# Kernel optimization log

Measured on AMD Instinct MI355X. Metric: run time of the kernel, lower is better.

The kernel has to match this reference:

```python
import jax, jax.numpy as jnp
import numpy as np

B, M, D, E, T, K = 16384, 6, 128, 6, 60, 2

def _gelu(x):
    return jax.nn.gelu(x, approximate=False)  # torch default exact GELU

def setup_inputs() -> dict:
    key = jax.random.key(0)
    ks = jax.random.split(key, 20)
    def p(k, shape, fan_in):
        return (jax.random.normal(k, shape, jnp.float32) / np.sqrt(fan_in)).astype(jnp.float32)
    inp = {
        "mode_features": jax.random.normal(ks[0], (B, M, D), jnp.float32),
        # router MLP: D->256->128->E
        "rW1": p(ks[1], (D, 256), D),   "rb1": jnp.zeros((256,), jnp.float32),
        "rW2": p(ks[2], (256, 128), 256), "rb2": jnp.zeros((128,), jnp.float32),
        "rW3": p(ks[3], (128, E), 128), "rb3": jnp.zeros((E,), jnp.float32),
        # stacked expert trajectory heads: D->256->256->T*2
        "tW1": p(ks[4], (E, D, 256), D),   "tb1": jnp.zeros((E, 256), jnp.float32),
        "tW2": p(ks[5], (E, 256, 256), 256), "tb2": jnp.zeros((E, 256), jnp.float32),
        "tW3": p(ks[6], (E, 256, T * 2), 256), "tb3": jnp.zeros((E, T * 2), jnp.float32),
        # stacked expert score heads: D->128->64->1
        "sW1": p(ks[7], (E, D, 128), D),  "sb1": jnp.zeros((E, 128), jnp.float32),
        "sW2": p(ks[8], (E, 128, 64), 128), "sb2": jnp.zeros((E, 64), jnp.float32),
        "sW3": p(ks[9], (E, 64, 1), 64), "sb3": jnp.zeros((E, 1), jnp.float32),
    }
    return inp

def reference(mode_features, rW1, rb1, rW2, rb2, rW3, rb3,
              tW1, tb1, tW2, tb2, tW3, tb3,
              sW1, sb1, sW2, sb2, sW3, sb3):
    b, m, d = mode_features.shape
    x = mode_features.reshape(b * m, d)  # [N, D]

    # Router (dropout is inference no-op)
    h = _gelu(x @ rW1 + rb1)
    h = _gelu(h @ rW2 + rb2)
    logits = (h @ rW3 + rb3).reshape(b, m, E)
    probs = jax.nn.softmax(logits, axis=-1)  # [B, M, E]

    # Top-2 sparse gating
    top_v, top_i = jax.lax.top_k(logits, K)          # [B, M, K]
    top_w = jax.nn.softmax(top_v, axis=-1)           # renormalized over top-k
    sparse_w = jnp.sum(jax.nn.one_hot(top_i, E, dtype=top_w.dtype) * top_w[..., None], axis=2)  # [B, M, E]

    # All-expert trajectory heads (dense redundant compute, as in source)
    ht = _gelu(jnp.einsum('nd,edh->neh', x, tW1) + tb1)
    ht = _gelu(jnp.einsum('neh,ehk->nek', ht, tW2) + tb2)
    traj = (jnp.einsum('nek,eko->neo', ht, tW3) + tb3).reshape(b, m, E, T, 2)

    # All-expert score heads
    hs = _gelu(jnp.einsum('nd,edh->neh', x, sW1) + sb1)
    hs = _gelu(jnp.einsum('neh,ehk->nek', hs, sW2) + sb2)
    score = (jnp.einsum('nek,eko->neo', hs, sW3) + sb3)[..., 0].reshape(b, m, E)

    trajectories = jnp.einsum('bmeto,bme->bmto', traj, sparse_w)  # [B, M, T, 2]
    scores = jnp.einsum('bme,bme->bm', score, sparse_w)           # [B, M]

    avg = probs.reshape(b * m, E).mean(axis=0)
    aux_loss = E * jnp.sum(avg * avg)
    return trajectories, scores, aux_loss, probs
```

## Files before the change

### kernel.cpp

```cpp
#include <hip/hip_runtime.h>
#include <math.h>

#define N_TOK  98304
#define NE     6
#define NPAIR  36
#define TCOL   120
#define RMARGIN 1.0e-3f

#define WS_SE    0
#define WS_CNT   32
#define WS_CUR   192
#define WS_BAS   352
#define WS_RCNT  504
#define WS_TB    512
#define WS_PAIR  1024
#define WS_W1A   394240
#define WS_W2A   787456
#define WS_LIST  1180672
#define WS_RW1T  1573888
#define WS_RW3T  1704960
#define WS_FRAG  1708032
#define WS_RFRAG 3575808

#define EOFF      155648
#define FOFF_TW1  0
#define FOFF_TW2  32768
#define FOFF_TW3  98304
#define FOFF_SW1  131072
#define FOFF_SW2  147456

#define RF_W1HI 0
#define RF_W1LO 32768
#define RF_W2HI 65536
#define RF_W2LO 98304
#define RF_W3HI 131072
#define RF_W3LO 133120

#define XS_OFF   0
#define HS1_OFF  17408
#define H2_OFF   0
#define H1_OFF   34816
#define HS2_OFF  68608
#define TOK_OFF  77824
#define WA_OFF   78080
#define WB_OFF   78336
#define SC_OFF   78592
#define SM_BYTES 78848

#define RXHI  0
#define RXLO  8704
#define RH2HI 0
#define RH2LO 8704
#define RH1HI 17408
#define RH1LO 34304
#define RLG   51200
#define SRED  52224
#define RSM_BYTES 52256

typedef short short8 __attribute__((ext_vector_type(8)));
typedef float f32x4  __attribute__((ext_vector_type(4)));

__device__ __forceinline__ short f2bf(float f) {
  unsigned int u = __builtin_bit_cast(unsigned int, f);
  u = u + 0x7FFFu + ((u >> 16) & 1u);
  return (short)(u >> 16);
}
__device__ __forceinline__ float bf2f(short s) {
  unsigned int u = ((unsigned int)(unsigned short)s) << 16;
  return __builtin_bit_cast(float, u);
}
__device__ __forceinline__ float gelu_exact(float x) {
  return 0.5f * x * (1.0f + erff(x * 0.7071067811865476f));
}
__device__ __forceinline__ float gelu_fast(float x) {
  float x2 = x * x;
  float u  = x * fmaf(0.1029454f, x2, 2.3021188f);
  float d  = 1.0f + exp2f(-u);
  return x * __builtin_amdgcn_rcpf(d);
}

__global__ __launch_bounds__(256) void k_prep(
    const float* __restrict__ rW1, const float* __restrict__ rW2,
    const float* __restrict__ rW3,
    const float* __restrict__ tW1, const float* __restrict__ tW2,
    const float* __restrict__ tW3, const float* __restrict__ sW1,
    const float* __restrict__ sW2, char* __restrict__ ws)
{
  const int tid = threadIdx.x, blk = blockIdx.x;
  const int lane = tid & 63, l15 = lane & 15, quad = lane >> 4;
  if (blk < 456) {
    const int g = blk * 4 + (tid >> 6);
    const int e = g / 304, r = g - e * 304;
    const float* src; int KT, Nreal, dstoff, nt, kt;
    if (r < 64)       { KT=4; src=tW1+e*32768; Nreal=256; dstoff=FOFF_TW1; kt=r&3;        nt=r>>2; }
    else if (r < 192) { int r2=r-64;  KT=8; src=tW2+e*65536; Nreal=256; dstoff=FOFF_TW2; kt=r2&7; nt=r2>>3; }
    else if (r < 256) { int r2=r-192; KT=8; src=tW3+e*30720; Nreal=120; dstoff=FOFF_TW3; kt=r2&7; nt=r2>>3; }
    else if (r < 288) { int r2=r-256; KT=4; src=sW1+e*16384; Nreal=128; dstoff=FOFF_SW1; kt=r2&3; nt=r2>>2; }
    else              { int r2=r-288; KT=4; src=sW2+e*8192;  Nreal=64;  dstoff=FOFF_SW2; kt=r2&3; nt=r2>>2; }
    const int n = nt * 16 + l15;
    short8 v;
    #pragma unroll
    for (int j = 0; j < 8; ++j) {
      int k = kt * 32 + quad * 8 + j;
      float f = (n < Nreal) ? src[k * Nreal + n] : 0.f;
      v[j] = f2bf(f);
    }
    short* dst = (short*)(ws + WS_FRAG) + (size_t)e * EOFF + dstoff + (nt * KT + kt) * 512 + lane * 8;
    *(short8*)dst = v;
  } else if (blk < 489) {
    const int g = (blk - 456) * 4 + (tid >> 6);
    const float* src; int KT, Nreal, kt, nt, dhi, dlo;
    if (g < 64)       { KT=4; src=rW1; Nreal=256; kt=g&3; nt=g>>2; dhi=RF_W1HI; dlo=RF_W1LO; }
    else if (g < 128) { int g2=g-64; KT=8; src=rW2; Nreal=128; kt=g2&7; nt=g2>>3; dhi=RF_W2HI; dlo=RF_W2LO; }
    else              { int g2=g-128; KT=4; src=rW3; Nreal=6;  kt=g2;   nt=0;     dhi=RF_W3HI; dlo=RF_W3LO; }
    const int n = nt * 16 + l15;
    short8 vh, vl;
    #pragma unroll
    for (int j = 0; j < 8; ++j) {
      int k = kt * 32 + quad * 8 + j;
      float f = (n < Nreal) ? src[k * Nreal + n] : 0.f;
      short hi = f2bf(f);
      vh[j] = hi;
      vl[j] = f2bf(f - bf2f(hi));
    }
    short* base = (short*)(ws + WS_RFRAG);
    const int idx = (nt * KT + kt) * 512 + lane * 8;
    *(short8*)(base + dhi + idx) = vh;
    *(short8*)(base + dlo + idx) = vl;
  } else {
    const int t = (blk - 489) * 256 + tid;
    if (t < 32768) {
      int c = t >> 7, k = t & 127;
      ((float*)(ws + WS_RW1T))[t] = rW1[k * 256 + c];
    } else if (t < 33536) {
      int t2 = t - 32768, e = t2 >> 7, j = t2 & 127;
      ((float*)(ws + WS_RW3T))[t2] = rW3[j * 6 + e];
    }
  }
}

__global__ __launch_bounds__(256) void k_router2(
    const float* __restrict__ xg,
    const float* __restrict__ b1, const float* __restrict__ b2,
    const float* __restrict__ b3,
    float* __restrict__ probs_out, char* __restrict__ ws)
{
  __shared__ __attribute__((aligned(16))) char sm[RSM_BYTES];
  const int tid = threadIdx.x;
  const int lane = tid & 63, w = tid >> 6;
  const int l15 = lane & 15, quad = lane >> 4;
  const int tok0 = blockIdx.x * 32;
  const short* rf = (const short*)(ws + WS_RFRAG);
  const f32x4 z = {0.f, 0.f, 0.f, 0.f};

  if (tid < NE) ((float*)(sm + SRED))[tid] = 0.f;

  {
    const int t = tid >> 3, seg = tid & 7;
    const float4* src = (const float4*)(xg + (size_t)(tok0 + t) * 128 + seg * 16);
    unsigned int* dhi = (unsigned int*)((short*)(sm + RXHI) + t * 136 + seg * 16);
    unsigned int* dlo = (unsigned int*)((short*)(sm + RXLO) + t * 136 + seg * 16);
    #pragma unroll
    for (int i = 0; i < 4; ++i) {
      float4 v = src[i];
      float f0=v.x, f1=v.y, f2=v.z, f3=v.w;
      short h0=f2bf(f0), h1=f2bf(f1), h2=f2bf(f2), h3=f2bf(f3);
      short o0=f2bf(f0-bf2f(h0)), o1=f2bf(f1-bf2f(h1)), o2=f2bf(f2-bf2f(h2)), o3=f2bf(f3-bf2f(h3));
      dhi[i*2+0] = (unsigned int)(unsigned short)h0 | ((unsigned int)(unsigned short)h1 << 16);
      dhi[i*2+1] = (unsigned int)(unsigned short)h2 | ((unsigned int)(unsigned short)h3 << 16);
      dlo[i*2+0] = (unsigned int)(unsigned short)o0 | ((unsigned int)(unsigned short)o1 << 16);
      dlo[i*2+1] = (unsigned int)(unsigned short)o2 | ((unsigned int)(unsigned short)o3 << 16);
    }
  }
  __syncthreads();

  {
    f32x4 acc[2][4];
    #pragma unroll
    for (int mt = 0; mt < 2; ++mt)
      #pragma unroll
      for (int ntl = 0; ntl < 4; ++ntl) acc[mt][ntl] = z;
    #pragma unroll
    for (int kt = 0; kt < 4; ++kt) {
      short8 ahi[2], alo[2];
      #pragma unroll
      for (int mt = 0; mt < 2; ++mt) {
        const int ro = (mt * 16 + l15) * 136 + kt * 32 + quad * 8;
        ahi[mt] = *(const short8*)((short*)(sm + RXHI) + ro);
        alo[mt] = *(const short8*)((short*)(sm + RXLO) + ro);
      }
      #pragma unroll
      for (int ntl = 0; ntl < 4; ++ntl) {
        const int nt = w * 4 + ntl;
        const int fi = (nt * 4 + kt) * 512 + lane * 8;
        short8 bhi = *(const short8*)(rf + RF_W1HI + fi);
        short8 blo = *(const short8*)(rf + RF_W1LO + fi);
        #pragma unroll
        for (int mt = 0; mt < 2; ++mt) {
          acc[mt][ntl] = __builtin_amdgcn_mfma_f32_16x16x32_bf16(ahi[mt], bhi, acc[mt][ntl], 0, 0, 0);
          acc[mt][ntl] = __builtin_amdgcn_mfma_f32_16x16x32_bf16(ahi[mt], blo, acc[mt][ntl], 0, 0, 0);
          acc[mt][ntl] = __builtin_amdgcn_mfma_f32_16x16x32_bf16(alo[mt], bhi, acc[mt][ntl], 0, 0, 0);
        }
      }
    }
    #pragma unroll
    for (int ntl = 0; ntl < 4; ++ntl) {
      const int n = (w * 4 + ntl) * 16 + l15;
      const float bv = b1[n];
      #pragma unroll
      for (int mt = 0; mt < 2; ++mt) {
        #pragma unroll
        for (int i = 0; i < 4; ++i) {
          const int r = mt * 16 + quad * 4 + i;
          float f = gelu_exact(acc[mt][ntl][i] + bv);
          short hi = f2bf(f);
          ((short*)(sm + RH1HI))[r * 264 + n] = hi;
          ((short*)(sm + RH1LO))[r * 264 + n] = f2bf(f - bf2f(hi));
        }
      }
    }
  }
  __syncthreads();

  {
    f32x4 acc[2][2];
    #pragma unroll
    for (int mt = 0; mt < 2; ++mt) { acc[mt][0] = z; acc[mt][1] = z; }
    #pragma unroll
    for (int kt = 0; kt < 8; ++kt) {
      short8 ahi[2], alo[2];
      #pragma unroll
      for (int mt = 0; mt < 2; ++mt) {
        const int ro = (mt * 16 + l15) * 264 + kt * 32 + quad * 8;
        ahi[mt] = *(const short8*)((short*)(sm + RH1HI) + ro);
        alo[mt] = *(const short8*)((short*)(sm + RH1LO) + ro);
      }
      #pragma unroll
      for (int ntl = 0; ntl < 2; ++ntl) {
        const int nt = w * 2 + ntl;
        const int fi = (nt * 8 + kt) * 512 + lane * 8;
        short8 bhi = *(const short8*)(rf + RF_W2HI + fi);
        short8 blo = *(const short8*)(rf + RF_W2LO + fi);
        #pragma unroll
        for (int mt = 0; mt < 2; ++mt) {
          acc[mt][ntl] = __builtin_amdgcn_mfma_f32_16x16x32_bf16(ahi[mt], bhi, acc[mt][ntl], 0, 0, 0);
          acc[mt][ntl] = __builtin_amdgcn_mfma_f32_16x16x32_bf16(ahi[mt], blo, acc[mt][ntl], 0, 0, 0);
          acc[mt][ntl] = __builtin_amdgcn_mfma_f32_16x16x32_bf16(alo[mt], bhi, acc[mt][ntl], 0, 0, 0);
        }
      }
    }
    #pragma unroll
    for (int ntl = 0; ntl < 2; ++ntl) {
      const int n = (w * 2 + ntl) * 16 + l15;
      const float bv = b2[n];
      #pragma unroll
      for (int mt = 0; mt < 2; ++mt) {
        #pragma unroll
        for (int i = 0; i < 4; ++i) {
          const int r = mt * 16 + quad * 4 + i;
          float f = gelu_exact(acc[mt][ntl][i] + bv);
          short hi = f2bf(f);
          ((short*)(sm + RH2HI))[r * 136 + n] = hi;
          ((short*)(sm + RH2LO))[r * 136 + n] = f2bf(f - bf2f(hi));
        }
      }
    }
  }
  __syncthreads();

  if (w < 2) {
    f32x4 acc = z;
    #pragma unroll
    for (int kt = 0; kt < 4; ++kt) {
      const int ro = (w * 16 + l15) * 136 + kt * 32 + quad * 8;
      short8 ahi = *(const short8*)((short*)(sm + RH2HI) + ro);
      short8 alo = *(const short8*)((short*)(sm + RH2LO) + ro);
      const int fi = kt * 512 + lane * 8;
      short8 bhi = *(const short8*)(rf + RF_W3HI + fi);
      short8 blo = *(const short8*)(rf + RF_W3LO + fi);
      acc = __builtin_amdgcn_mfma_f32_16x16x32_bf16(ahi, bhi, acc, 0, 0, 0);
      acc = __builtin_amdgcn_mfma_f32_16x16x32_bf16(ahi, blo, acc, 0, 0, 0);
      acc = __builtin_amdgcn_mfma_f32_16x16x32_bf16(alo, bhi, acc, 0, 0, 0);
    }
    if (l15 < NE) {
      const float bv = b3[l15];
      #pragma unroll
      for (int i = 0; i < 4; ++i) {
        const int r = w * 16 + quad * 4 + i;
        ((float*)(sm + RLG))[r * 8 + l15] = acc[i] + bv;
      }
    }
  }
  __syncthreads();

  if (tid < 32) {
    const int n = tok0 + tid;
    float l[NE];
    #pragma unroll
    for (int e = 0; e < NE; ++e) l[e] = ((float*)(sm + RLG))[tid * 8 + e];
    int e1 = 0; float v1 = l[0];
    #pragma unroll
    for (int e = 1; e < NE; ++e) if (l[e] > v1) { v1 = l[e]; e1 = e; }
    int e2 = -1; float v2 = -3.4e38f;
    #pragma unroll
    for (int e = 0; e < NE; ++e) if (e != e1 && l[e] > v2) { v2 = l[e]; e2 = e; }
    float v3 = -3.4e38f;
    #pragma unroll
    for (int e = 0; e < NE; ++e) if (e != e1 && e != e2 && l[e] > v3) v3 = l[e];

    float ew = expf(v2 - v1);
    float winv = 1.f / (1.f + ew);
    ((unsigned int*)(ws + WS_PAIR))[n] = (unsigned int)e1 | ((unsigned int)e2 << 8);
    ((float*)(ws + WS_W1A))[n] = winv;
    ((float*)(ws + WS_W2A))[n] = ew * winv;

    float s = 0.f;
    #pragma unroll
    for (int e = 0; e < NE; ++e) { l[e] = expf(l[e] - v1); s += l[e]; }
    float inv = 1.f / s;
    float* po = probs_out + (size_t)n * NE;
    #pragma unroll
    for (int e = 0; e < NE; ++e) {
      l[e] *= inv; po[e] = l[e];
      atomicAdd((float*)(sm + SRED) + e, l[e]);
    }
    if (v2 - v3 < RMARGIN) {
      int idx = atomicAdd((int*)(ws + WS_RCNT), 1);
      ((int*)(ws + WS_LIST))[idx] = n;
    }
  }
  __syncthreads();
  if (tid < NE) atomicAdd((float*)(ws + WS_SE) + tid, ((float*)(sm + SRED))[tid]);
}

__global__ __launch_bounds__(256) void k_repair(
    const float* __restrict__ xg,
    const float* __restrict__ b1, const float* __restrict__ rW2,
    const float* __restrict__ b2, const float* __restrict__ b3,
    float* __restrict__ probs_out, char* __restrict__ ws)
{
  __shared__ float xs[4][128], h1b[4][256], h2b[4][128], lgb[4][8];
  const int tid = threadIdx.x, lane = tid & 63, w = tid >> 6;
  const int gw = blockIdx.x * 4 + w, NW = gridDim.x * 4;
  const int rc = *(const int*)(ws + WS_RCNT);
  const float* w1t = (const float*)(ws + WS_RW1T);
  const float* w3t = (const float*)(ws + WS_RW3T);

  for (int i = gw; i < rc; i += NW) {
    const int n = ((const int*)(ws + WS_LIST))[i];
    xs[w][lane]      = xg[(size_t)n * 128 + lane];
    xs[w][64 + lane] = xg[(size_t)n * 128 + 64 + lane];
    __builtin_amdgcn_s_waitcnt(0);
    #pragma unroll 1
    for (int c4 = 0; c4 < 4; ++c4) {
      const int c = c4 * 64 + lane;
      float acc = b1[c];
      const float* wr = w1t + c * 128;
      #pragma unroll
      for (int k = 0; k < 128; ++k) acc = fmaf(xs[w][k], wr[k], acc);
      h1b[w][c] = gelu_exact(acc);
    }
    __builtin_amdgcn_s_waitcnt(0);
    #pragma unroll 1
    for (int c2 = 0; c2 < 2; ++c2) {
      const int c = c2 * 64 + lane;
      float acc = b2[c];
      #pragma unroll 4
      for (int k = 0; k < 256; ++k) acc = fmaf(h1b[w][k], rW2[k * 128 + c], acc);
      h2b[w][c] = gelu_exact(acc);
    }
    __builtin_amdgcn_s_waitcnt(0);
    if (lane < NE) {
      float acc = b3[lane];
      const float* wr = w3t + lane * 128;
      #pragma unroll
      for (int k = 0; k < 128; ++k) acc = fmaf(h2b[w][k], wr[k], acc);
      lgb[w][lane] = acc;
    }
    __builtin_amdgcn_s_waitcnt(0);
    if (lane == 0) {
      float l[NE];
      #pragma unroll
      for (int e = 0; e < NE; ++e) l[e] = lgb[w][e];
      int e1 = 0; float v1 = l[0];
      #pragma unroll
      for (int e = 1; e < NE; ++e) if (l[e] > v1) { v1 = l[e]; e1 = e; }
      int e2 = -1; float v2 = -3.4e38f;
      #pragma unroll
      for (int e = 0; e < NE; ++e) if (e != e1 && l[e] > v2) { v2 = l[e]; e2 = e; }
      float ew = expf(v2 - v1);
      float winv = 1.f / (1.f + ew);
      ((unsigned int*)(ws + WS_PAIR))[n] = (unsigned int)e1 | ((unsigned int)e2 << 8);
      ((float*)(ws + WS_W1A))[n] = winv;
      ((float*)(ws + WS_W2A))[n] = ew * winv;
      float s = 0.f;
      #pragma unroll
      for (int e = 0; e < NE; ++e) { l[e] = expf(l[e] - v1); s += l[e]; }
      float inv = 1.f / s;
      float* po = probs_out + (size_t)n * NE;
      #pragma unroll
      for (int e = 0; e < NE; ++e) po[e] = l[e] * inv;
    }
  }
}

__global__ __launch_bounds__(256) void k_count(char* __restrict__ ws)
{
  __shared__ int lcnt[NPAIR];
  const int tid = threadIdx.x;
  if (tid < NPAIR) lcnt[tid] = 0;
  __syncthreads();
  const int n = blockIdx.x * 256 + tid;
  unsigned int pr = ((const unsigned int*)(ws + WS_PAIR))[n];
  atomicAdd(&lcnt[(int)(pr & 255u) * NE + (int)((pr >> 8) & 255u)], 1);
  __syncthreads();
  if (tid < NPAIR && lcnt[tid]) atomicAdd((int*)(ws + WS_CNT) + tid, lcnt[tid]);
}

__global__ void k_scan(char* __restrict__ ws, float* __restrict__ aux_out)
{
  if (threadIdx.x == 0 && blockIdx.x == 0) {
    int* cnt = (int*)(ws + WS_CNT);
    int* cur = (int*)(ws + WS_CUR);
    int* bas = (int*)(ws + WS_BAS);
    int* tb  = (int*)(ws + WS_TB);
    int s = 0, ts = 0;
    for (int p = 0; p < NPAIR; ++p) {
      bas[p] = s; cur[p] = s; tb[p] = ts;
      s  += cnt[p];
      ts += (cnt[p] + 63) >> 6;
    }
    bas[NPAIR] = s; tb[NPAIR] = ts;
    const float* Se = (const float*)(ws + WS_SE);
    float a = 0.f;
    for (int e = 0; e < NE; ++e) { float m = Se[e] * (1.f / (float)N_TOK); a += m * m; }
    *aux_out = (float)NE * a;
  }
}

__global__ __launch_bounds__(256) void k_place(char* __restrict__ ws)
{
  __shared__ int lcnt[NPAIR], lbase[NPAIR];
  const int tid = threadIdx.x;
  if (tid < NPAIR) lcnt[tid] = 0;
  __syncthreads();
  const int n = blockIdx.x * 256 + tid;
  unsigned int pr = ((const unsigned int*)(ws + WS_PAIR))[n];
  const int p = (int)(pr & 255u) * NE + (int)((pr >> 8) & 255u);
  int loc = atomicAdd(&lcnt[p], 1);
  __syncthreads();
  if (tid < NPAIR && lcnt[tid]) lbase[tid] = atomicAdd((int*)(ws + WS_CUR) + tid, lcnt[tid]);
  __syncthreads();
  ((int*)(ws + WS_LIST))[lbase[p] + loc] = n;
}

template<int KTILES, int NTW>
__device__ __forceinline__ void gemm_phase(
    const char* sm, int aOff, int aStride,
    const short* __restrict__ bfrag, int ntBase,
    f32x4 (&acc)[4][NTW], int lane)
{
  const int l15 = lane & 15, quad = lane >> 4;
  #pragma unroll
  for (int kt = 0; kt < KTILES; ++kt) {
    short8 a[4];
    #pragma unroll
    for (int mt = 0; mt < 4; ++mt) {
      const short* ap = (const short*)(sm + aOff) + (mt * 16 + l15) * aStride + kt * 32 + quad * 8;
      a[mt] = *(const short8*)ap;
    }
    #pragma unroll
    for (int ntl = 0; ntl < NTW; ++ntl) {
      const int nt = ntBase + ntl;
      short8 b = *(const short8*)(bfrag + (size_t)(nt * KTILES + kt) * 512 + lane * 8);
      #pragma unroll
      for (int mt = 0; mt < 4; ++mt)
        acc[mt][ntl] = __builtin_amdgcn_mfma_f32_16x16x32_bf16(a[mt], b, acc[mt][ntl], 0, 0, 0);
    }
  }
}

template<int NTW>
__device__ __forceinline__ void epi_gelu(
    char* sm, int outOff, int outStride, const float* __restrict__ bias,
    f32x4 (&acc)[4][NTW], int ntBase, int lane)
{
  const int l15 = lane & 15, quad = lane >> 4;
  #pragma unroll
  for (int ntl = 0; ntl < NTW; ++ntl) {
    const int n = (ntBase + ntl) * 16 + l15;
    float bv = bias[n];
    #pragma unroll
    for (int mt = 0; mt < 4; ++mt) {
      #pragma unroll
      for (int i = 0; i < 4; ++i) {
        const int r = mt * 16 + quad * 4 + i;
        ((short*)(sm + outOff))[r * outStride + n] = f2bf(gelu_fast(acc[mt][ntl][i] + bv));
      }
    }
  }
}

__global__ __launch_bounds__(256, 2) void k_expert(
    const float* __restrict__ xg,
    const float* __restrict__ tb1, const float* __restrict__ tb2, const float* __restrict__ tb3,
    const float* __restrict__ sb1, const float* __restrict__ sb2, const float* __restrict__ sb3,
    const float* __restrict__ sw3,
    float* __restrict__ traj_out, float* __restrict__ sc_out,
    const char* __restrict__ ws)
{
  __shared__ __attribute__((aligned(16))) char sm[SM_BYTES];
  const int tid  = threadIdx.x;
  const int lane = tid & 63, w = tid >> 6;
  const int l15  = lane & 15, quad = lane >> 4;

  const int* tb = (const int*)(ws + WS_TB);
  const int b = blockIdx.x;
  if (b >= tb[NPAIR]) return;
  int p = 0;
  #pragma unroll 1
  for (int q = 1; q < NPAIR; ++q) if (b >= tb[q]) p = q;
  const int t = b - tb[p];
  const int* bas = (const int*)(ws + WS_BAS);
  const int segbase = bas[p];
  const int cnt = bas[p + 1] - segbase;
  const int e1 = p / NE, e2 = p - e1 * NE;

  int* tokv = (int*)(sm + TOK_OFF);
  if (tid < 64) {
    const int o = t * 64 + tid;
    const bool valid = o < cnt;
    int tok = valid ? ((const int*)(ws + WS_LIST))[segbase + o] : -1;
    tokv[tid] = tok;
    ((float*)(sm + WA_OFF))[tid] = valid ? ((const float*)(ws + WS_W1A))[tok] : 0.f;
    ((float*)(sm + WB_OFF))[tid] = valid ? ((const float*)(ws + WS_W2A))[tok] : 0.f;
  }
  __syncthreads();

  const short* fragw = (const short*)(ws + WS_FRAG);
  const f32x4 z = {0.f, 0.f, 0.f, 0.f};
  f32x4 tacc[4][2];
  #pragma unroll
  for (int mt = 0; mt < 4; ++mt) { tacc[mt][0] = z; tacc[mt][1] = z; }

  #pragma unroll 1
  for (int s = 0; s < 2; ++s) {
    const int e = s ? e2 : e1;
    const short* fb = fragw + (size_t)e * EOFF;
    const int woff = s ? WB_OFF : WA_OFF;

    {
      const int r = tid >> 2, seg = tid & 3;
      int tok = tokv[r]; if (tok < 0) tok = 0;
      const float4* src = (const float4*)(xg + (size_t)tok * 128 + seg * 32);
      short* dst = (short*)(sm + XS_OFF) + r * 136 + seg * 32;
      #pragma unroll
      for (int i = 0; i < 8; ++i) {
        float4 v = src[i];
        unsigned int a = (unsigned int)(unsigned short)f2bf(v.x) | ((unsigned int)(unsigned short)f2bf(v.y) << 16);
        unsigned int c = (unsigned int)(unsigned short)f2bf(v.z) | ((unsigned int)(unsigned short)f2bf(v.w) << 16);
        ((unsigned int*)dst)[i * 2 + 0] = a;
        ((unsigned int*)dst)[i * 2 + 1] = c;
      }
    }
    __syncthreads();

    {
      f32x4 acc[4][2];
      #pragma unroll
      for (int mt = 0; mt < 4; ++mt) { acc[mt][0] = z; acc[mt][1] = z; }
      gemm_phase<4, 2>(sm, XS_OFF, 136, fb + FOFF_SW1, w * 2, acc, lane);
      epi_gelu<2>(sm, HS1_OFF, 136, sb1 + e * 128, acc, w * 2, lane);
    }
    __syncthreads();

    {
      f32x4 acc[4][1];
      #pragma unroll
      for (int mt = 0; mt < 4; ++mt) acc[mt][0] = z;
      gemm_phase<4, 1>(sm, HS1_OFF, 136, fb + FOFF_SW2, w, acc, lane);
      epi_gelu<1>(sm, HS2_OFF, 72, sb2 + e * 64, acc, w, lane);
    }
    __syncthreads();

    if (tid < 64) {
      const short* h = (const short*)(sm + HS2_OFF) + tid * 72;
      const float* w3e = sw3 + e * 64;
      float acc = 0.f;
      #pragma unroll
      for (int kk = 0; kk < 8; ++kk) {
        short8 v8 = *(const short8*)(h + kk * 8);
        #pragma unroll
        for (int j = 0; j < 8; ++j) acc = fmaf(bf2f(v8[j]), w3e[kk * 8 + j], acc);
      }
      acc += sb3[e];
      float c = ((float*)(sm + woff))[tid] * acc;
      float* scl = (float*)(sm + SC_OFF);
      if (s == 0) scl[tid] = c; else scl[tid] += c;
    }

    {
      f32x4 acc[4][4];
      #pragma unroll
      for (int mt = 0; mt < 4; ++mt)
        #pragma unroll
        for (int ntl = 0; ntl < 4; ++ntl) acc[mt][ntl] = z;
      gemm_phase<4, 4>(sm, XS_OFF, 136, fb + FOFF_TW1, w * 4, acc, lane);
      epi_gelu<4>(sm, H1_OFF, 264, tb1 + e * 256, acc, w * 4, lane);
    }
    __syncthreads();

    {
      f32x4 acc[4][4];
      #pragma unroll
      for (int mt = 0; mt < 4; ++mt)
        #pragma unroll
        for (int ntl = 0; ntl < 4; ++ntl) acc[mt][ntl] = z;
      gemm_phase<8, 4>(sm, H1_OFF, 264, fb + FOFF_TW2, w * 4, acc, lane);
      epi_gelu<4>(sm, H2_OFF, 264, tb2 + e * 256, acc, w * 4, lane);
    }
    __syncthreads();

    {
      f32x4 acc[4][2];
      #pragma unroll
      for (int mt = 0; mt < 4; ++mt) { acc[mt][0] = z; acc[mt][1] = z; }
      gemm_phase<8, 2>(sm, H2_OFF, 264, fb + FOFF_TW3, w * 2, acc, lane);
      const float* wl = (const float*)(sm + woff);
      f32x4 wv[4];
      #pragma unroll
      for (int mt = 0; mt < 4; ++mt) wv[mt] = *(const f32x4*)(wl + mt * 16 + quad * 4);
      #pragma unroll
      for (int ntl = 0; ntl < 2; ++ntl) {
        const int nn = (w * 2 + ntl) * 16 + l15;
        float bv = (nn < TCOL) ? tb3[e * TCOL + nn] : 0.f;
        #pragma unroll
        for (int mt = 0; mt < 4; ++mt)
          #pragma unroll
          for (int i = 0; i < 4; ++i)
            tacc[mt][ntl][i] += wv[mt][i] * (acc[mt][ntl][i] + bv);
      }
    }
    __syncthreads();
  }

  #pragma unroll
  for (int ntl = 0; ntl < 2; ++ntl) {
    const int nn = (w * 2 + ntl) * 16 + l15;
    if (nn < TCOL) {
      #pragma unroll
      for (int mt = 0; mt < 4; ++mt) {
        #pragma unroll
        for (int i = 0; i < 4; ++i) {
          const int r = mt * 16 + quad * 4 + i;
          const int tok = tokv[r];
          if (tok >= 0) traj_out[(size_t)tok * TCOL + nn] = tacc[mt][ntl][i];
        }
      }
    }
  }
  if (tid < 64) {
    const int tok = tokv[tid];
    if (tok >= 0) sc_out[tok] = ((float*)(sm + SC_OFF))[tid];
  }
}

extern "C" void kernel_launch(void* const* d_in, const int* in_sizes, int n_in,
                              void* d_out, int out_size, void* d_ws, size_t ws_size,
                              hipStream_t stream)
{
  const float* x   = (const float*)d_in[0];
  const float* rW1 = (const float*)d_in[1];  const float* rb1 = (const float*)d_in[2];
  const float* rW2 = (const float*)d_in[3];  const float* rb2 = (const float*)d_in[4];
  const float* rW3 = (const float*)d_in[5];  const float* rb3 = (const float*)d_in[6];
  const float* tW1 = (const float*)d_in[7];  const float* tb1 = (const float*)d_in[8];
  const float* tW2 = (const float*)d_in[9];  const float* tb2 = (const float*)d_in[10];
  const float* tW3 = (const float*)d_in[11]; const float* tb3 = (const float*)d_in[12];
  const float* sW1 = (const float*)d_in[13]; const float* sb1 = (const float*)d_in[14];
  const float* sW2 = (const float*)d_in[15]; const float* sb2 = (const float*)d_in[16];
  const float* sW3 = (const float*)d_in[17]; const float* sb3 = (const float*)d_in[18];
  char* ws = (char*)d_ws;
  float* out    = (float*)d_out;
  float* traj   = out;
  float* scores = out + 11796480;
  float* aux    = out + 11894784;
  float* probs  = out + 11894785;

  hipMemsetAsync(d_ws, 0, 512, stream);

  hipLaunchKernelGGL(k_prep, dim3(620), dim3(256), 0, stream,
                     rW1, rW2, rW3, tW1, tW2, tW3, sW1, sW2, ws);

  hipLaunchKernelGGL(k_router2, dim3(N_TOK / 32), dim3(256), 0, stream,
                     x, rb1, rb2, rb3, probs, ws);

  hipLaunchKernelGGL(k_repair, dim3(256), dim3(256), 0, stream,
                     x, rb1, rW2, rb2, rb3, probs, ws);

  hipLaunchKernelGGL(k_count, dim3(N_TOK / 256), dim3(256), 0, stream, ws);

  hipLaunchKernelGGL(k_scan, dim3(1), dim3(64), 0, stream, ws, aux);

  hipLaunchKernelGGL(k_place, dim3(N_TOK / 256), dim3(256), 0, stream, ws);

  hipLaunchKernelGGL(k_expert, dim3(1600), dim3(256), 0, stream,
                     x, tb1, tb2, tb3, sb1, sb2, sb3, sW3, traj, scores, ws);
}
```

Measured before the change: 465.7 us.

## Drop split-bf16 router precision and shrink expert LDS to fit three blocks

The router GEMMs stop using hi/lo bf16 splitting and plain bf16 MFMA replaces the three-pass product. The re-check margin for near-tied top-2 logits is widened so more tokens go through the fp32 repair kernel. The expert kernel computes the 256-wide first trajectory layer in two 128-column halves that reuse one smaller LDS buffer. It also accumulates layer 2 across both halves and splits layer 3 over two buffers, cutting LDS so launch bounds can target three blocks per CU. The trade-off is extra barriers, fewer tokens per MFMA reuse, more repair work, and lower router accuracy.

```diff
diff --git a/kernel.cpp b/kernel.cpp
--- a/kernel.cpp
+++ b/kernel.cpp
@@ -5,7 +5,7 @@
 #define NE     6
 #define NPAIR  36
 #define TCOL   120
-#define RMARGIN 1.0e-3f
+#define RMARGIN 0.06f
 
 #define WS_SE    0
 #define WS_CNT   32
@@ -29,33 +29,24 @@
 #define FOFF_SW1  131072
 #define FOFF_SW2  147456
 
-#define RF_W1HI 0
-#define RF_W1LO 32768
-#define RF_W2HI 65536
-#define RF_W2LO 98304
-#define RF_W3HI 131072
-#define RF_W3LO 133120
+#define RF_W1 0
+#define RF_W2 32768
+#define RF_W3 65536
 
 #define XS_OFF   0
-#define HS1_OFF  17408
-#define H2_OFF   0
-#define H1_OFF   34816
-#define HS2_OFF  68608
-#define TOK_OFF  77824
-#define WA_OFF   78080
-#define WB_OFF   78336
-#define SC_OFF   78592
-#define SM_BYTES 78848
-
-#define RXHI  0
-#define RXLO  8704
-#define RH2HI 0
-#define RH2LO 8704
-#define RH1HI 17408
-#define RH1LO 34304
-#define RLG   51200
-#define SRED  52224
-#define RSM_BYTES 52256
+#define BUF_OFF  17408
+#define HS2_OFF  34816
+#define TOK_OFF  44032
+#define WA_OFF   44288
+#define WB_OFF   44544
+#define SC_OFF   44800
+#define SM_BYTES 45056
+
+#define RX_OFF   0
+#define RH1_OFF  8704
+#define RLG_OFF  25600
+#define RSRED    26624
+#define RSM_BYTES 26656
 
 typedef short short8 __attribute__((ext_vector_type(8)));
 typedef float f32x4  __attribute__((ext_vector_type(4)));
@@ -109,24 +100,19 @@
     *(short8*)dst = v;
   } else if (blk < 489) {
     const int g = (blk - 456) * 4 + (tid >> 6);
-    const float* src; int KT, Nreal, kt, nt, dhi, dlo;
-    if (g < 64)       { KT=4; src=rW1; Nreal=256; kt=g&3; nt=g>>2; dhi=RF_W1HI; dlo=RF_W1LO; }
-    else if (g < 128) { int g2=g-64; KT=8; src=rW2; Nreal=128; kt=g2&7; nt=g2>>3; dhi=RF_W2HI; dlo=RF_W2LO; }
-    else              { int g2=g-128; KT=4; src=rW3; Nreal=6;  kt=g2;   nt=0;     dhi=RF_W3HI; dlo=RF_W3LO; }
+    const float* src; int KT, Nreal, kt, nt, doff;
+    if (g < 64)       { KT=4; src=rW1; Nreal=256; kt=g&3; nt=g>>2; doff=RF_W1; }
+    else if (g < 128) { int g2=g-64;  KT=8; src=rW2; Nreal=128; kt=g2&7; nt=g2>>3; doff=RF_W2; }
+    else              { int g2=g-128; KT=4; src=rW3; Nreal=6;   kt=g2;   nt=0;     doff=RF_W3; }
     const int n = nt * 16 + l15;
-    short8 vh, vl;
+    short8 v;
     #pragma unroll
     for (int j = 0; j < 8; ++j) {
       int k = kt * 32 + quad * 8 + j;
       float f = (n < Nreal) ? src[k * Nreal + n] : 0.f;
-      short hi = f2bf(f);
-      vh[j] = hi;
-      vl[j] = f2bf(f - bf2f(hi));
-    }
-    short* base = (short*)(ws + WS_RFRAG);
-    const int idx = (nt * KT + kt) * 512 + lane * 8;
-    *(short8*)(base + dhi + idx) = vh;
-    *(short8*)(base + dlo + idx) = vl;
+      v[j] = f2bf(f);
+    }
+    *(short8*)((short*)(ws + WS_RFRAG) + doff + (nt * KT + kt) * 512 + lane * 8) = v;
   } else {
     const int t = (blk - 489) * 256 + tid;
     if (t < 32768) {
@@ -139,6 +125,52 @@
   }
 }
 
+template<int MT, int KT, int NTW, int BST>
+__device__ __forceinline__ void gemm_g(
+    const char* sm, int aOff, int aStride,
+    const short* __restrict__ bfrag, int ntBase,
+    f32x4 (&acc)[MT][NTW], int lane)
+{
+  const int l15 = lane & 15, quad = lane >> 4;
+  #pragma unroll
+  for (int kt = 0; kt < KT; ++kt) {
+    short8 a[MT];
+    #pragma unroll
+    for (int mt = 0; mt < MT; ++mt) {
+      const short* ap = (const short*)(sm + aOff) + (mt * 16 + l15) * aStride + kt * 32 + quad * 8;
+      a[mt] = *(const short8*)ap;
+    }
+    #pragma unroll
+    for (int ntl = 0; ntl < NTW; ++ntl) {
+      short8 b = *(const short8*)(bfrag + (size_t)((ntBase + ntl) * BST + kt) * 512 + lane * 8);
+      #pragma unroll
+      for (int mt = 0; mt < MT; ++mt)
+        acc[mt][ntl] = __builtin_amdgcn_mfma_f32_16x16x32_bf16(a[mt], b, acc[mt][ntl], 0, 0, 0);
+    }
+  }
+}
+
+template<int MT, int NTW>
+__device__ __forceinline__ void epi_gelu(
+    char* sm, int outOff, int outStride, const float* __restrict__ bias,
+    f32x4 (&acc)[MT][NTW], int ntBase, int lane)
+{
+  const int l15 = lane & 15, quad = lane >> 4;
+  #pragma unroll
+  for (int ntl = 0; ntl < NTW; ++ntl) {
+    const int n = (ntBase + ntl) * 16 + l15;
+    float bv = bias[n];
+    #pragma unroll
+    for (int mt = 0; mt < MT; ++mt) {
+      #pragma unroll
+      for (int i = 0; i < 4; ++i) {
+        const int r = mt * 16 + quad * 4 + i;
+        ((short*)(sm + outOff))[r * outStride + n] = f2bf(gelu_fast(acc[mt][ntl][i] + bv));
+      }
+    }
+  }
+}
+
 __global__ __launch_bounds__(256) void k_router2(
     const float* __restrict__ xg,
     const float* __restrict__ b1, const float* __restrict__ b2,
@@ -153,23 +185,17 @@
   const short* rf = (const short*)(ws + WS_RFRAG);
   const f32x4 z = {0.f, 0.f, 0.f, 0.f};
 
-  if (tid < NE) ((float*)(sm + SRED))[tid] = 0.f;
+  if (tid < NE) ((float*)(sm + RSRED))[tid] = 0.f;
 
   {
     const int t = tid >> 3, seg = tid & 7;
     const float4* src = (const float4*)(xg + (size_t)(tok0 + t) * 128 + seg * 16);
-    unsigned int* dhi = (unsigned int*)((short*)(sm + RXHI) + t * 136 + seg * 16);
-    unsigned int* dlo = (unsigned int*)((short*)(sm + RXLO) + t * 136 + seg * 16);
+    unsigned int* dst = (unsigned int*)((short*)(sm + RX_OFF) + t * 136 + seg * 16);
     #pragma unroll
     for (int i = 0; i < 4; ++i) {
       float4 v = src[i];
-      float f0=v.x, f1=v.y, f2=v.z, f3=v.w;
-      short h0=f2bf(f0), h1=f2bf(f1), h2=f2bf(f2), h3=f2bf(f3);
-      short o0=f2bf(f0-bf2f(h0)), o1=f2bf(f1-bf2f(h1)), o2=f2bf(f2-bf2f(h2)), o3=f2bf(f3-bf2f(h3));
-      dhi[i*2+0] = (unsigned int)(unsigned short)h0 | ((unsigned int)(unsigned short)h1 << 16);
-      dhi[i*2+1] = (unsigned int)(unsigned short)h2 | ((unsigned int)(unsigned short)h3 << 16);
-      dlo[i*2+0] = (unsigned int)(unsigned short)o0 | ((unsigned int)(unsigned short)o1 << 16);
-      dlo[i*2+1] = (unsigned int)(unsigned short)o2 | ((unsigned int)(unsigned short)o3 << 16);
+      dst[i*2+0] = (unsigned int)(unsigned short)f2bf(v.x) | ((unsigned int)(unsigned short)f2bf(v.y) << 16);
+      dst[i*2+1] = (unsigned int)(unsigned short)f2bf(v.z) | ((unsigned int)(unsigned short)f2bf(v.w) << 16);
     }
   }
   __syncthreads();
@@ -180,45 +206,8 @@
     for (int mt = 0; mt < 2; ++mt)
       #pragma unroll
       for (int ntl = 0; ntl < 4; ++ntl) acc[mt][ntl] = z;
-    #pragma unroll
-    for (int kt = 0; kt < 4; ++kt) {
-      short8 ahi[2], alo[2];
-      #pragma unroll
-      for (int mt = 0; mt < 2; ++mt) {
-        const int ro = (mt * 16 + l15) * 136 + kt * 32 + quad * 8;
-        ahi[mt] = *(const short8*)((short*)(sm + RXHI) + ro);
-        alo[mt] = *(const short8*)((short*)(sm + RXLO) + ro);
-      }
-      #pragma unroll
-      for (int ntl = 0; ntl < 4; ++ntl) {
-        const int nt = w * 4 + ntl;
-        const int fi = (nt * 4 + kt) * 512 + lane * 8;
-        short8 bhi = *(const short8*)(rf + RF_W1HI + fi);
-        short8 blo = *(const short8*)(rf + RF_W1LO + fi);
-        #pragma unroll
-        for (int mt = 0; mt < 2; ++mt) {
-          acc[mt][ntl] = __builtin_amdgcn_mfma_f32_16x16x32_bf16(ahi[mt], bhi, acc[mt][ntl], 0, 0, 0);
-          acc[mt][ntl] = __builtin_amdgcn_mfma_f32_16x16x32_bf16(ahi[mt], blo, acc[mt][ntl], 0, 0, 0);
-          acc[mt][ntl] = __builtin_amdgcn_mfma_f32_16x16x32_bf16(alo[mt], bhi, acc[mt][ntl], 0, 0, 0);
-        }
-      }
-    }
-    #pragma unroll
-    for (int ntl = 0; ntl < 4; ++ntl) {
-      const int n = (w * 4 + ntl) * 16 + l15;
-      const float bv = b1[n];
-      #pragma unroll
-      for (int mt = 0; mt < 2; ++mt) {
-        #pragma unroll
-        for (int i = 0; i < 4; ++i) {
-          const int r = mt * 16 + quad * 4 + i;
-          float f = gelu_exact(acc[mt][ntl][i] + bv);
-          short hi = f2bf(f);
-          ((short*)(sm + RH1HI))[r * 264 + n] = hi;
-          ((short*)(sm + RH1LO))[r * 264 + n] = f2bf(f - bf2f(hi));
-        }
-      }
-    }
+    gemm_g<2, 4, 4, 4>(sm, RX_OFF, 136, rf + RF_W1, w * 4, acc, lane);
+    epi_gelu<2, 4>(sm, RH1_OFF, 264, b1, acc, w * 4, lane);
   }
   __syncthreads();
 
@@ -226,68 +215,20 @@
     f32x4 acc[2][2];
     #pragma unroll
     for (int mt = 0; mt < 2; ++mt) { acc[mt][0] = z; acc[mt][1] = z; }
-    #pragma unroll
-    for (int kt = 0; kt < 8; ++kt) {
-      short8 ahi[2], alo[2];
-      #pragma unroll
-      for (int mt = 0; mt < 2; ++mt) {
-        const int ro = (mt * 16 + l15) * 264 + kt * 32 + quad * 8;
-        ahi[mt] = *(const short8*)((short*)(sm + RH1HI) + ro);
-        alo[mt] = *(const short8*)((short*)(sm + RH1LO) + ro);
-      }
-      #pragma unroll
-      for (int ntl = 0; ntl < 2; ++ntl) {
-        const int nt = w * 2 + ntl;
-        const int fi = (nt * 8 + kt) * 512 + lane * 8;
-        short8 bhi = *(const short8*)(rf + RF_W2HI + fi);
-        short8 blo = *(const short8*)(rf + RF_W2LO + fi);
-        #pragma unroll
-        for (int mt = 0; mt < 2; ++mt) {
-          acc[mt][ntl] = __builtin_amdgcn_mfma_f32_16x16x32_bf16(ahi[mt], bhi, acc[mt][ntl], 0, 0, 0);
-          acc[mt][ntl] = __builtin_amdgcn_mfma_f32_16x16x32_bf16(ahi[mt], blo, acc[mt][ntl], 0, 0, 0);
-          acc[mt][ntl] = __builtin_amdgcn_mfma_f32_16x16x32_bf16(alo[mt], bhi, acc[mt][ntl], 0, 0, 0);
-        }
-      }
-    }
-    #pragma unroll
-    for (int ntl = 0; ntl < 2; ++ntl) {
-      const int n = (w * 2 + ntl) * 16 + l15;
-      const float bv = b2[n];
-      #pragma unroll
-      for (int mt = 0; mt < 2; ++mt) {
-        #pragma unroll
-        for (int i = 0; i < 4; ++i) {
-          const int r = mt * 16 + quad * 4 + i;
-          float f = gelu_exact(acc[mt][ntl][i] + bv);
-          short hi = f2bf(f);
-          ((short*)(sm + RH2HI))[r * 136 + n] = hi;
-          ((short*)(sm + RH2LO))[r * 136 + n] = f2bf(f - bf2f(hi));
-        }
-      }
-    }
+    gemm_g<2, 8, 2, 8>(sm, RH1_OFF, 264, rf + RF_W2, w * 2, acc, lane);
+    epi_gelu<2, 2>(sm, RX_OFF, 136, b2, acc, w * 2, lane);
   }
   __syncthreads();
 
   if (w < 2) {
-    f32x4 acc = z;
-    #pragma unroll
-    for (int kt = 0; kt < 4; ++kt) {
-      const int ro = (w * 16 + l15) * 136 + kt * 32 + quad * 8;
-      short8 ahi = *(const short8*)((short*)(sm + RH2HI) + ro);
-      short8 alo = *(const short8*)((short*)(sm + RH2LO) + ro);
-      const int fi = kt * 512 + lane * 8;
-      short8 bhi = *(const short8*)(rf + RF_W3HI + fi);
-      short8 blo = *(const short8*)(rf + RF_W3LO + fi);
-      acc = __builtin_amdgcn_mfma_f32_16x16x32_bf16(ahi, bhi, acc, 0, 0, 0);
-      acc = __builtin_amdgcn_mfma_f32_16x16x32_bf16(ahi, blo, acc, 0, 0, 0);
-      acc = __builtin_amdgcn_mfma_f32_16x16x32_bf16(alo, bhi, acc, 0, 0, 0);
-    }
+    f32x4 acc[1][1]; acc[0][0] = z;
+    gemm_g<1, 4, 1, 4>(sm, RX_OFF + w * 16 * 136 * 2, 136, rf + RF_W3, 0, acc, lane);
     if (l15 < NE) {
       const float bv = b3[l15];
       #pragma unroll
       for (int i = 0; i < 4; ++i) {
         const int r = w * 16 + quad * 4 + i;
-        ((float*)(sm + RLG))[r * 8 + l15] = acc[i] + bv;
+        ((float*)(sm + RLG_OFF))[r * 8 + l15] = acc[0][0][i] + bv;
       }
     }
   }
@@ -297,7 +238,7 @@
     const int n = tok0 + tid;
     float l[NE];
     #pragma unroll
-    for (int e = 0; e < NE; ++e) l[e] = ((float*)(sm + RLG))[tid * 8 + e];
+    for (int e = 0; e < NE; ++e) l[e] = ((float*)(sm + RLG_OFF))[tid * 8 + e];
     int e1 = 0; float v1 = l[0];
     #pragma unroll
     for (int e = 1; e < NE; ++e) if (l[e] > v1) { v1 = l[e]; e1 = e; }
@@ -322,7 +263,7 @@
     #pragma unroll
     for (int e = 0; e < NE; ++e) {
       l[e] *= inv; po[e] = l[e];
-      atomicAdd((float*)(sm + SRED) + e, l[e]);
+      atomicAdd((float*)(sm + RSRED) + e, l[e]);
     }
     if (v2 - v3 < RMARGIN) {
       int idx = atomicAdd((int*)(ws + WS_RCNT), 1);
@@ -330,7 +271,7 @@
     }
   }
   __syncthreads();
-  if (tid < NE) atomicAdd((float*)(ws + WS_SE) + tid, ((float*)(sm + SRED))[tid]);
+  if (tid < NE) atomicAdd((float*)(ws + WS_SE) + tid, ((float*)(sm + RSRED))[tid]);
 }
 
 __global__ __launch_bounds__(256) void k_repair(
@@ -351,21 +292,21 @@
     xs[w][lane]      = xg[(size_t)n * 128 + lane];
     xs[w][64 + lane] = xg[(size_t)n * 128 + 64 + lane];
     __builtin_amdgcn_s_waitcnt(0);
-    #pragma unroll 1
+    #pragma unroll
     for (int c4 = 0; c4 < 4; ++c4) {
       const int c = c4 * 64 + lane;
       float acc = b1[c];
       const float* wr = w1t + c * 128;
-      #pragma unroll
+      #pragma unroll 8
       for (int k = 0; k < 128; ++k) acc = fmaf(xs[w][k], wr[k], acc);
       h1b[w][c] = gelu_exact(acc);
     }
     __builtin_amdgcn_s_waitcnt(0);
-    #pragma unroll 1
+    #pragma unroll
     for (int c2 = 0; c2 < 2; ++c2) {
       const int c = c2 * 64 + lane;
       float acc = b2[c];
-      #pragma unroll 4
+      #pragma unroll 8
       for (int k = 0; k < 256; ++k) acc = fmaf(h1b[w][k], rW2[k * 128 + c], acc);
       h2b[w][c] = gelu_exact(acc);
     }
@@ -373,7 +314,7 @@
     if (lane < NE) {
       float acc = b3[lane];
       const float* wr = w3t + lane * 128;
-      #pragma unroll
+      #pragma unroll 8
       for (int k = 0; k < 128; ++k) acc = fmaf(h2b[w][k], wr[k], acc);
       lgb[w][lane] = acc;
     }
@@ -454,54 +395,7 @@
   ((int*)(ws + WS_LIST))[lbase[p] + loc] = n;
 }
 
-template<int KTILES, int NTW>
-__device__ __forceinline__ void gemm_phase(
-    const char* sm, int aOff, int aStride,
-    const short* __restrict__ bfrag, int ntBase,
-    f32x4 (&acc)[4][NTW], int lane)
-{
-  const int l15 = lane & 15, quad = lane >> 4;
-  #pragma unroll
-  for (int kt = 0; kt < KTILES; ++kt) {
-    short8 a[4];
-    #pragma unroll
-    for (int mt = 0; mt < 4; ++mt) {
-      const short* ap = (const short*)(sm + aOff) + (mt * 16 + l15) * aStride + kt * 32 + quad * 8;
-      a[mt] = *(const short8*)ap;
-    }
-    #pragma unroll
-    for (int ntl = 0; ntl < NTW; ++ntl) {
-      const int nt = ntBase + ntl;
-      short8 b = *(const short8*)(bfrag + (size_t)(nt * KTILES + kt) * 512 + lane * 8);
-      #pragma unroll
-      for (int mt = 0; mt < 4; ++mt)
-        acc[mt][ntl] = __builtin_amdgcn_mfma_f32_16x16x32_bf16(a[mt], b, acc[mt][ntl], 0, 0, 0);
-    }
-  }
-}
-
-template<int NTW>
-__device__ __forceinline__ void epi_gelu(
-    char* sm, int outOff, int outStride, const float* __restrict__ bias,
-    f32x4 (&acc)[4][NTW], int ntBase, int lane)
-{
-  const int l15 = lane & 15, quad = lane >> 4;
-  #pragma unroll
-  for (int ntl = 0; ntl < NTW; ++ntl) {
-    const int n = (ntBase + ntl) * 16 + l15;
-    float bv = bias[n];
-    #pragma unroll
-    for (int mt = 0; mt < 4; ++mt) {
-      #pragma unroll
-      for (int i = 0; i < 4; ++i) {
-        const int r = mt * 16 + quad * 4 + i;
-        ((short*)(sm + outOff))[r * outStride + n] = f2bf(gelu_fast(acc[mt][ntl][i] + bv));
-      }
-    }
-  }
-}
-
-__global__ __launch_bounds__(256, 2) void k_expert(
+__global__ __launch_bounds__(256, 3) void k_expert(
     const float* __restrict__ xg,
     const float* __restrict__ tb1, const float* __restrict__ tb2, const float* __restrict__ tb3,
     const float* __restrict__ sb1, const float* __restrict__ sb2, const float* __restrict__ sb3,
@@ -553,14 +447,12 @@
       const int r = tid >> 2, seg = tid & 3;
       int tok = tokv[r]; if (tok < 0) tok = 0;
       const float4* src = (const float4*)(xg + (size_t)tok * 128 + seg * 32);
-      short* dst = (short*)(sm + XS_OFF) + r * 136 + seg * 32;
+      unsigned int* dst = (unsigned int*)((short*)(sm + XS_OFF) + r * 136 + seg * 32);
       #pragma unroll
       for (int i = 0; i < 8; ++i) {
         float4 v = src[i];
-        unsigned int a = (unsigned int)(unsigned short)f2bf(v.x) | ((unsigned int)(unsigned short)f2bf(v.y) << 16);
-        unsigned int c = (unsigned int)(unsigned short)f2bf(v.z) | ((unsigned int)(unsigned short)f2bf(v.w) << 16);
-        ((unsigned int*)dst)[i * 2 + 0] = a;
-        ((unsigned int*)dst)[i * 2 + 1] = c;
+        dst[i*2+0] = (unsigned int)(unsigned short)f2bf(v.x) | ((unsigned int)(unsigned short)f2bf(v.y) << 16);
+        dst[i*2+1] = (unsigned int)(unsigned short)f2bf(v.z) | ((unsigned int)(unsigned short)f2bf(v.w) << 16);
       }
     }
     __syncthreads();
@@ -569,8 +461,8 @@
       f32x4 acc[4][2];
       #pragma unroll
       for (int mt = 0; mt < 4; ++mt) { acc[mt][0] = z; acc[mt][1] = z; }
-      gemm_phase<4, 2>(sm, XS_OFF, 136, fb + FOFF_SW1, w * 2, acc, lane);
-      epi_gelu<2>(sm, HS1_OFF, 136, sb1 + e * 128, acc, w * 2, lane);
+      gemm_g<4, 4, 2, 4>(sm, XS_OFF, 136, fb + FOFF_SW1, w * 2, acc, lane);
+      epi_gelu<4, 2>(sm, BUF_OFF, 136, sb1 + e * 128, acc, w * 2, lane);
     }
     __syncthreads();
 
@@ -578,46 +470,8 @@
       f32x4 acc[4][1];
       #pragma unroll
       for (int mt = 0; mt < 4; ++mt) acc[mt][0] = z;
-      gemm_phase<4, 1>(sm, HS1_OFF, 136, fb + FOFF_SW2, w, acc, lane);
-      epi_gelu<1>(sm, HS2_OFF, 72, sb2 + e * 64, acc, w, lane);
-    }
-    __syncthreads();
-
-    if (tid < 64) {
-      const short* h = (const short*)(sm + HS2_OFF) + tid * 72;
-      const float* w3e = sw3 + e * 64;
-      float acc = 0.f;
-      #pragma unroll
-      for (int kk = 0; kk < 8; ++kk) {
-        short8 v8 = *(const short8*)(h + kk * 8);
-        #pragma unroll
-        for (int j = 0; j < 8; ++j) acc = fmaf(bf2f(v8[j]), w3e[kk * 8 + j], acc);
-      }
-      acc += sb3[e];
-      float c = ((float*)(sm + woff))[tid] * acc;
-      float* scl = (float*)(sm + SC_OFF);
-      if (s == 0) scl[tid] = c; else scl[tid] += c;
-    }
-
-    {
-      f32x4 acc[4][4];
-      #pragma unroll
-      for (int mt = 0; mt < 4; ++mt)
-        #pragma unroll
-        for (int ntl = 0; ntl < 4; ++ntl) acc[mt][ntl] = z;
-      gemm_phase<4, 4>(sm, XS_OFF, 136, fb + FOFF_TW1, w * 4, acc, lane);
-      epi_gelu<4>(sm, H1_OFF, 264, tb1 + e * 256, acc, w * 4, lane);
-    }
-    __syncthreads();
-
-    {
-      f32x4 acc[4][4];
-      #pragma unroll
-      for (int mt = 0; mt < 4; ++mt)
-        #pragma unroll
-        for (int ntl = 0; ntl < 4; ++ntl) acc[mt][ntl] = z;
-      gemm_phase<8, 4>(sm, H1_OFF, 264, fb + FOFF_TW2, w * 4, acc, lane);
-      epi_gelu<4>(sm, H2_OFF, 264, tb2 + e * 256, acc, w * 4, lane);
+      gemm_g<4, 4, 1, 4>(sm, BUF_OFF, 136, fb + FOFF_SW2, w, acc, lane);
+      epi_gelu<4, 1>(sm, HS2_OFF, 72, sb2 + e * 64, acc, w, lane);
     }
     __syncthreads();
 
@@ -625,7 +479,77 @@
       f32x4 acc[4][2];
       #pragma unroll
       for (int mt = 0; mt < 4; ++mt) { acc[mt][0] = z; acc[mt][1] = z; }
-      gemm_phase<8, 2>(sm, H2_OFF, 264, fb + FOFF_TW3, w * 2, acc, lane);
+      gemm_g<4, 4, 2, 4>(sm, XS_OFF, 136, fb + FOFF_TW1, w * 2, acc, lane);
+      {
+        const int r = tid >> 2, kq = tid & 3;
+        const short* h = (const short*)(sm + HS2_OFF) + r * 72 + kq * 16;
+        const float* w3e = sw3 + e * 64 + kq * 16;
+        float sacc = 0.f;
+        #pragma unroll
+        for (int kk = 0; kk < 2; ++kk) {
+          short8 v8 = *(const short8*)(h + kk * 8);
+          #pragma unroll
+          for (int j = 0; j < 8; ++j) sacc = fmaf(bf2f(v8[j]), w3e[kk * 8 + j], sacc);
+        }
+        sacc += __shfl_xor(sacc, 1);
+        sacc += __shfl_xor(sacc, 2);
+        if (kq == 0) {
+          float c = ((float*)(sm + woff))[r] * (sacc + sb3[e]);
+          float* scl = (float*)(sm + SC_OFF);
+          if (s == 0) scl[r] = c; else scl[r] += c;
+        }
+      }
+      epi_gelu<4, 2>(sm, BUF_OFF, 136, tb1 + e * 256, acc, w * 2, lane);
+    }
+    __syncthreads();
+
+    f32x4 acc2[4][4];
+    #pragma unroll
+    for (int mt = 0; mt < 4; ++mt)
+      #pragma unroll
+      for (int ntl = 0; ntl < 4; ++ntl) acc2[mt][ntl] = z;
+
+    gemm_g<4, 4, 4, 8>(sm, BUF_OFF, 136, fb + FOFF_TW2, w * 4, acc2, lane);
+    __syncthreads();
+
+    {
+      f32x4 acc[4][2];
+      #pragma unroll
+      for (int mt = 0; mt < 4; ++mt) { acc[mt][0] = z; acc[mt][1] = z; }
+      gemm_g<4, 4, 2, 4>(sm, XS_OFF, 136, fb + FOFF_TW1 + 8 * 4 * 512, w * 2, acc, lane);
+      epi_gelu<4, 2>(sm, BUF_OFF, 136, tb1 + e * 256 + 128, acc, w * 2, lane);
+    }
+    __syncthreads();
+
+    gemm_g<4, 4, 4, 8>(sm, BUF_OFF, 136, fb + FOFF_TW2 + 4 * 512, w * 4, acc2, lane);
+    __syncthreads();
+
+    {
+      const float* bb = tb2 + e * 256;
+      #pragma unroll
+      for (int ntl = 0; ntl < 4; ++ntl) {
+        const int n = (w * 4 + ntl) * 16 + l15;
+        const float bv = bb[n];
+        #pragma unroll
+        for (int mt = 0; mt < 4; ++mt) {
+          #pragma unroll
+          for (int i = 0; i < 4; ++i) {
+            const int r = mt * 16 + quad * 4 + i;
+            short vbf = f2bf(gelu_fast(acc2[mt][ntl][i] + bv));
+            if (n < 128) ((short*)(sm + XS_OFF))[r * 136 + n] = vbf;
+            else         ((short*)(sm + BUF_OFF))[r * 136 + (n - 128)] = vbf;
+          }
+        }
+      }
+    }
+    __syncthreads();
+
+    {
+      f32x4 acc3[4][2];
+      #pragma unroll
+      for (int mt = 0; mt < 4; ++mt) { acc3[mt][0] = z; acc3[mt][1] = z; }
+      gemm_g<4, 4, 2, 8>(sm, XS_OFF, 136, fb + FOFF_TW3, w * 2, acc3, lane);
+      gemm_g<4, 4, 2, 8>(sm, BUF_OFF, 136, fb + FOFF_TW3 + 4 * 512, w * 2, acc3, lane);
       const float* wl = (const float*)(sm + woff);
       f32x4 wv[4];
       #pragma unroll
@@ -638,7 +562,7 @@
         for (int mt = 0; mt < 4; ++mt)
           #pragma unroll
           for (int i = 0; i < 4; ++i)
-            tacc[mt][ntl][i] += wv[mt][i] * (acc[mt][ntl][i] + bv);
+            tacc[mt][ntl][i] += wv[mt][i] * (acc3[mt][ntl][i] + bv);
       }
     }
     __syncthreads();
```

Result: slower. 1.191 ms (+155.8%).
